# Optimization experiments

Hardware: AMD Instinct MI355X
Metric: run time of the kernel (lower is better)

## Reference

```python
import jax, jax.numpy as jnp
import numpy as np

B, NFIELD = 8192, 20
NFEAT = 100000
SQL_VOCAB = NFIELD + NFEAT + 1  # 100021
SQL_NEMB, DATA_NEMB = 16, 64
HID = 1024
OUT = 1
K = 16
ALPHA = 1.5
N_BISECT = 50


def entmax_bisect(x, alpha=ALPHA, n_iter=N_BISECT):
    # alpha-entmax via bisection on the threshold tau (Peters et al. 2019).
    am1 = alpha - 1.0
    x = x * am1
    d = x.shape[-1]
    max_val = jnp.max(x, axis=-1, keepdims=True)
    tau_lo = max_val - 1.0
    tau_hi = max_val - d ** (1.0 - alpha)

    def p(tau):
        return jnp.clip(x - tau, 0.0) ** (1.0 / am1)

    f_lo = jnp.sum(p(tau_lo), axis=-1, keepdims=True) - 1.0

    def body(carry, _):
        tau_lo, tau_hi, f_lo = carry
        tau_m = 0.5 * (tau_lo + tau_hi)
        f_m = jnp.sum(p(tau_m), axis=-1, keepdims=True) - 1.0
        same_side = (f_m * f_lo) >= 0
        tau_lo = jnp.where(same_side, tau_m, tau_lo)
        tau_hi = jnp.where(same_side, tau_hi, tau_m)
        f_lo = jnp.where(same_side, f_m, f_lo)
        return (tau_lo, tau_hi, f_lo), None

    (tau_lo, tau_hi, _), _ = jax.lax.scan(body, (tau_lo, tau_hi, f_lo), None, length=n_iter)
    pm = p(0.5 * (tau_lo + tau_hi))
    return pm / jnp.sum(pm, axis=-1, keepdims=True)


def cv_squared(v):
    eps = 1e-10
    var = jnp.var(v, ddof=1)  # torch .var() is unbiased
    mean = jnp.mean(v)
    return var / (mean * mean + eps)


def setup_inputs() -> dict:
    key = jax.random.key(0)
    ks = jax.random.split(key, 12)
    xavier = lambda k, shp: jax.random.uniform(k, shp, jnp.float32, -1.0, 1.0) * jnp.sqrt(6.0 / (shp[-2] + shp[-1]))
    inp = {
        "x": jax.random.randint(ks[0], (B, NFIELD), 0, NFEAT),
        "sql": jax.random.randint(ks[1], (B, NFIELD), 0, SQL_VOCAB),
        "sql_emb_table": xavier(ks[2], (SQL_VOCAB, SQL_NEMB)),
        "input_emb_table": xavier(ks[3], (NFEAT, DATA_NEMB)),
        # gate: Linear(gate_in, HID) -> ReLU -> Linear(HID, K)
        "gW1": xavier(ks[4], (NFIELD * SQL_NEMB, HID)),
        "gb1": jnp.zeros((HID,), jnp.float32),
        "gW2": xavier(ks[5], (HID, K)),
        "gb2": jnp.zeros((K,), jnp.float32),
        # K experts: Linear(in, HID) -> ReLU -> Linear(HID, OUT), stacked on axis 0
        "eW1": xavier(ks[6], (K, NFIELD * DATA_NEMB, HID)),
        "eb1": jnp.zeros((K, HID), jnp.float32),
        "eW2": xavier(ks[7], (K, HID, OUT)),
        "eb2": jnp.zeros((K, OUT), jnp.float32),
    }
    return inp


def reference(x, sql, sql_emb_table, input_emb_table, gW1, gb1, gW2, gb2, eW1, eb1, eW2, eb2):
    Bn = x.shape[0]
    x_emb = input_emb_table[x].reshape(Bn, -1)      # [B, nfield*data_nemb]
    sql_emb = sql_emb_table[sql].reshape(Bn, -1)    # [B, nfield*sql_nemb]

    # gate network + entmax-bisect (dropout is identity in eval)
    g = jax.nn.relu(sql_emb @ gW1 + gb1) @ gW2 + gb2  # [B, K]
    gate_score = entmax_bisect(g)                     # [B, K], sparse simplex

    loss = cv_squared(jnp.sum(gate_score, axis=0))

    # all K experts on every token, vectorized
    h = jax.nn.relu(jnp.einsum("bi,kih->bkh", x_emb, eW1) + eb1)  # [B, K, HID]
    y_k = jnp.einsum("bkh,kho->bko", h, eW2) + eb2                # [B, K, OUT]
    y = jnp.sum(gate_score[:, :, None] * y_k, axis=1)             # [B, OUT]
    return (y.squeeze(-1), loss)
```

## Files before the change

### kernel.cpp

```cpp
#include <hip/hip_runtime.h>
#include <stdint.h>

#define NFIELD 20
#define HID 1024
#define KEXP 16
#define KX 1280
#define KS 320
#define BATCH 8192

typedef __bf16 bf16x8 __attribute__((ext_vector_type(8)));
typedef float f32x4 __attribute__((ext_vector_type(4)));

__device__ __forceinline__ unsigned short f2bf(float f) {
  union { float f; unsigned u; } v; v.f = f;
  unsigned r = v.u + 0x7FFFu + ((v.u >> 16) & 1u);
  return (unsigned short)(r >> 16);
}

__device__ __forceinline__ void gload16(const void* g, void* l) {
  __builtin_amdgcn_global_load_lds(
      (const __attribute__((address_space(1))) unsigned int*)(uintptr_t)g,
      (__attribute__((address_space(3))) unsigned int*)(unsigned)(uintptr_t)l,
      16, 0, 0);
}

#define SBAR() asm volatile("s_barrier" ::: "memory")


__global__ void transpose_cvt(const float* __restrict__ src, unsigned short* __restrict__ dst,
                              int R, int C, long sstride, long dstride) {
  __shared__ float tile[32][33];
  const float* s = src + (size_t)blockIdx.z * sstride;
  unsigned short* d = dst + (size_t)blockIdx.z * dstride;
  const int r0 = blockIdx.y * 32, c0 = blockIdx.x * 32;
  const int tx = threadIdx.x & 31, ty = threadIdx.x >> 5;
#pragma unroll
  for (int i = 0; i < 4; ++i)
    tile[ty + 8 * i][tx] = s[(size_t)(r0 + ty + 8 * i) * C + c0 + tx];
  __syncthreads();
#pragma unroll
  for (int i = 0; i < 4; ++i)
    d[(size_t)(c0 + ty + 8 * i) * R + r0 + tx] = f2bf(tile[tx][ty + 8 * i]);
}

__global__ void gather_x_k(const int* __restrict__ x, const float* __restrict__ tab,
                           unsigned short* __restrict__ out) {
  const int b = blockIdx.x;
  const int f = threadIdx.x >> 4;
  const int q = threadIdx.x & 15;
  const int idx = x[b * NFIELD + f];
  const float4 v = *(const float4*)(tab + (size_t)idx * 64 + q * 4);
  ushort4 o;
  o.x = f2bf(v.x); o.y = f2bf(v.y); o.z = f2bf(v.z); o.w = f2bf(v.w);
  *(ushort4*)(out + (size_t)b * KX + f * 64 + q * 4) = o;
}

__global__ void gather_sql_k(const int* __restrict__ sql, const float* __restrict__ tab,
                             unsigned short* __restrict__ out) {
  const int t = blockIdx.x * 256 + threadIdx.x;
  const int b = t / 80;
  const int r = t - b * 80;
  const int f = r >> 2, q = r & 3;
  const int idx = sql[b * NFIELD + f];
  const float4 v = *(const float4*)(tab + (size_t)idx * 16 + q * 4);
  ushort4 o;
  o.x = f2bf(v.x); o.y = f2bf(v.y); o.z = f2bf(v.z); o.w = f2bf(v.w);
  *(ushort4*)(out + (size_t)b * KS + f * 16 + q * 4) = o;
}

template <int NJO, int KTOT>
__global__ __launch_bounds__(256, 2) void gemm_k(const __bf16* __restrict__ A,
                                                 const __bf16* __restrict__ Bt,
                                                 const float* __restrict__ bias,
                                                 const float* __restrict__ W2,
                                                 float* __restrict__ out) {
  constexpr int NT = KTOT / 64;
  static_assert(NT >= 3, "pipeline needs NT>=3");
  alignas(16) __shared__ __bf16 As[2][128][64];
  alignas(16) __shared__ __bf16 Bs[2][128][64];

  const int tid = threadIdx.x;
  const int lane = tid & 63;
  const int wave = tid >> 6;
  const int wr = wave >> 1;
  const int wc = wave & 1;

  const unsigned f = blockIdx.y * gridDim.x + blockIdx.x;
  const unsigned nwg = gridDim.x * gridDim.y;
  const unsigned s = (f >> 3) + (f & 7u) * (nwg >> 3);
  const int m0 = (int)((s & 511u) >> 3) * 128;
  const int n0 = (int)((s >> 9) * 8 + (s & 7u)) * 128;

  const int srow = lane >> 3;
  const int sch = (lane & 7) ^ srow;
  const int r15 = lane & 15, g4 = lane >> 4;

  const __bf16* Ag = A + (size_t)(m0 + wave * 32 + srow) * KTOT + sch * 8;
  const __bf16* Bg = Bt + (size_t)(n0 + wave * 32 + srow) * KTOT + sch * 8;

  auto stage = [&](int t) {
    const int c = t & 1;
#pragma unroll
    for (int j = 0; j < 4; ++j)
      gload16(Ag + (size_t)(j * 8) * KTOT + t * 64, (void*)&As[c][wave * 32 + j * 8][0]);
#pragma unroll
    for (int j = 0; j < 4; ++j)
      gload16(Bg + (size_t)(j * 8) * KTOT + t * 64, (void*)&Bs[c][wave * 32 + j * 8][0]);
  };
  auto readfr = [&](int c, bf16x8 (&af)[4][2], bf16x8 (&bfr)[4][2]) {
#pragma unroll
    for (int mi = 0; mi < 4; ++mi) {
      const int row = wr * 64 + mi * 16 + r15;
#pragma unroll
      for (int kk = 0; kk < 2; ++kk)
        af[mi][kk] = *(const bf16x8*)&As[c][row][((kk * 4 + g4) ^ (row & 7)) * 8];
    }
#pragma unroll
    for (int ni = 0; ni < 4; ++ni) {
      const int row = wc * 64 + ni * 16 + r15;
#pragma unroll
      for (int kk = 0; kk < 2; ++kk)
        bfr[ni][kk] = *(const bf16x8*)&Bs[c][row][((kk * 4 + g4) ^ (row & 7)) * 8];
    }
  };

  f32x4 acc[4][4] = {};
  bf16x8 afA[4][2], bfA[4][2], afB[4][2], bfB[4][2];

#define MFMA16(AF, BF, KK)                                                     \
  __builtin_amdgcn_s_setprio(1);                                               \
  _Pragma("unroll") for (int mi = 0; mi < 4; ++mi)                             \
  _Pragma("unroll") for (int ni = 0; ni < 4; ++ni)                             \
      acc[mi][ni] = __builtin_amdgcn_mfma_f32_16x16x32_bf16(                   \
          AF[mi][KK], BF[ni][KK], acc[mi][ni], 0, 0, 0);                       \
  __builtin_amdgcn_s_setprio(0);

#define BODY(T, AFC, BFC, AFN, BFN)                                            \
  MFMA16(AFC, BFC, 0);                                                         \
  asm volatile("s_waitcnt lgkmcnt(0)" ::: "memory");                           \
  asm volatile("s_waitcnt vmcnt(0)" ::: "memory");                             \
  SBAR();                                                                      \
  if ((T) + 2 < NT) stage((T) + 2);                                            \
  readfr(((T) + 1) & 1, AFN, BFN);                                             \
  MFMA16(AFC, BFC, 1);                                                         \
  SBAR();

  stage(0);
  stage(1);
  asm volatile("s_waitcnt vmcnt(0)" ::: "memory");
  SBAR();
  readfr(0, afA, bfA);

  int t = 0;
  for (; t + 1 < NT - 1; t += 2) {
    BODY(t, afA, bfA, afB, bfB);
    BODY(t + 1, afB, bfB, afA, bfA);
  }
  if constexpr (((NT - 1) & 1) != 0) {
    BODY(NT - 2, afA, bfA, afB, bfB);
    MFMA16(afB, bfB, 0);
    MFMA16(afB, bfB, 1);
  } else {
    MFMA16(afA, bfA, 0);
    MFMA16(afA, bfA, 1);
  }
#undef BODY
#undef MFMA16

  int ncol[4];
  float bsv[4];
#pragma unroll
  for (int ni = 0; ni < 4; ++ni) {
    ncol[ni] = n0 + wc * 64 + ni * 16 + r15;
    bsv[ni] = bias[ncol[ni]];
  }
#pragma unroll
  for (int mi = 0; mi < 4; ++mi)
#pragma unroll
    for (int ni = 0; ni < 4; ++ni)
#pragma unroll
      for (int j = 0; j < 4; ++j) {
        float v = acc[mi][ni][j] + bsv[ni];
        acc[mi][ni][j] = v > 0.f ? v : 0.f;
      }
#pragma unroll
  for (int jo = 0; jo < NJO; ++jo) {
    float w4[4];
#pragma unroll
    for (int ni = 0; ni < 4; ++ni)
      w4[ni] = (NJO == 1) ? W2[ncol[ni]] : W2[ncol[ni] * NJO + jo];
#pragma unroll
    for (int mi = 0; mi < 4; ++mi)
#pragma unroll
      for (int j = 0; j < 4; ++j) {
        float s = acc[mi][0][j] * w4[0] + acc[mi][1][j] * w4[1] +
                  acc[mi][2][j] * w4[2] + acc[mi][3][j] * w4[3];
        s += __shfl_xor(s, 1);
        s += __shfl_xor(s, 2);
        s += __shfl_xor(s, 4);
        s += __shfl_xor(s, 8);
        if (r15 == 0) {
          const int row = m0 + wr * 64 + mi * 16 + g4 * 4 + j;
          const int oc = (NJO == 1) ? (n0 >> 10) : jo;
          atomicAdd(&out[row * KEXP + oc], s);
        }
      }
  }
}

__global__ void entmax_combine(const float* __restrict__ gacc, const float* __restrict__ gb2,
                               const float* __restrict__ yk, const float* __restrict__ eb2,
                               float* __restrict__ y, double* __restrict__ colsum) {
  const int b = blockIdx.x * 256 + threadIdx.x;
  float x[16];
  float mx = -3.4e38f;
#pragma unroll
  for (int j = 0; j < 16; ++j) {
    x[j] = (gacc[b * 16 + j] + gb2[j]) * 0.5f;
    mx = fmaxf(mx, x[j]);
  }
  float lo = mx - 1.0f, hi = mx - 0.25f;
  float flo = -1.0f;
#pragma unroll
  for (int j = 0; j < 16; ++j) {
    float d = x[j] - lo; d = d > 0.f ? d : 0.f;
    flo += d * d;
  }
  for (int it = 0; it < 50; ++it) {
    const float tm = 0.5f * (lo + hi);
    float fm = -1.0f;
#pragma unroll
    for (int j = 0; j < 16; ++j) {
      float d = x[j] - tm; d = d > 0.f ? d : 0.f;
      fm += d * d;
    }
    if (fm * flo >= 0.f) { lo = tm; flo = fm; } else { hi = tm; }
  }
  const float tm = 0.5f * (lo + hi);
  float p[16], ps = 0.f;
#pragma unroll
  for (int j = 0; j < 16; ++j) {
    float d = x[j] - tm; d = d > 0.f ? d : 0.f;
    p[j] = d * d; ps += p[j];
  }
  const float inv = 1.0f / ps;
  float yv = 0.f;
#pragma unroll
  for (int j = 0; j < 16; ++j) {
    p[j] *= inv;
    yv += p[j] * (yk[b * 16 + j] + eb2[j]);
  }
  y[b] = yv;

  const int lane = threadIdx.x & 63, wv = threadIdx.x >> 6;
  __shared__ float red[4][16];
#pragma unroll
  for (int j = 0; j < 16; ++j) {
    float v = p[j];
    v += __shfl_xor(v, 1);  v += __shfl_xor(v, 2);  v += __shfl_xor(v, 4);
    v += __shfl_xor(v, 8);  v += __shfl_xor(v, 16); v += __shfl_xor(v, 32);
    if (lane == 0) red[wv][j] = v;
  }
  __syncthreads();
  if (threadIdx.x < 16) {
    double s = (double)red[0][threadIdx.x] + (double)red[1][threadIdx.x] +
               (double)red[2][threadIdx.x] + (double)red[3][threadIdx.x];
    atomicAdd(&colsum[threadIdx.x], s);
  }
}

__global__ void loss_k(const double* __restrict__ colsum, float* __restrict__ out) {
  if (threadIdx.x == 0 && blockIdx.x == 0) {
    double m = 0.0;
    for (int k = 0; k < 16; ++k) m += colsum[k];
    m *= (1.0 / 16.0);
    double var = 0.0;
    for (int k = 0; k < 16; ++k) { const double d = colsum[k] - m; var += d * d; }
    var *= (1.0 / 15.0);
    out[0] = (float)(var / (m * m + 1e-10));
  }
}

extern "C" void kernel_launch(void* const* d_in, const int* in_sizes, int n_in,
                              void* d_out, int out_size, void* d_ws, size_t ws_size,
                              hipStream_t stream) {
  const int*   x    = (const int*)d_in[0];
  const int*   sql  = (const int*)d_in[1];
  const float* sqlT = (const float*)d_in[2];
  const float* inT  = (const float*)d_in[3];
  const float* gW1  = (const float*)d_in[4];
  const float* gb1  = (const float*)d_in[5];
  const float* gW2  = (const float*)d_in[6];
  const float* gb2  = (const float*)d_in[7];
  const float* eW1  = (const float*)d_in[8];
  const float* eb1  = (const float*)d_in[9];
  const float* eW2  = (const float*)d_in[10];
  const float* eb2  = (const float*)d_in[11];

  char* ws = (char*)d_ws;
  unsigned short* eW1T = (unsigned short*)(ws);
  unsigned short* xemb = (unsigned short*)(ws + 41943040);
  unsigned short* semb = (unsigned short*)(ws + 62914560);
  unsigned short* gW1T = (unsigned short*)(ws + 68157440);
  float*  yk     = (float*)(ws + 68812800);
  float*  gacc   = (float*)(ws + 69337088);
  double* colsum = (double*)(ws + 69861376);

  hipMemsetAsync(yk, 0, 524288 * 2 + 128, stream);

  transpose_cvt<<<dim3(32, 40, 16), 256, 0, stream>>>(eW1, eW1T, 1280, 1024, 1280L * 1024, 1024L * 1280);
  transpose_cvt<<<dim3(32, 10, 1), 256, 0, stream>>>(gW1, gW1T, 320, 1024, 0, 0);
  gather_x_k<<<BATCH, 320, 0, stream>>>(x, inT, xemb);
  gather_sql_k<<<BATCH * 80 / 256, 256, 0, stream>>>(sql, sqlT, semb);

  gemm_k<1, KX><<<dim3(16384 / 128, BATCH / 128), 256, 0, stream>>>(
      (const __bf16*)xemb, (const __bf16*)eW1T, eb1, eW2, yk);
  gemm_k<16, KS><<<dim3(HID / 128, BATCH / 128), 256, 0, stream>>>(
      (const __bf16*)semb, (const __bf16*)gW1T, gb1, gW2, gacc);

  entmax_combine<<<BATCH / 256, 256, 0, stream>>>(gacc, gb2, yk, eb2, (float*)d_out, colsum);
  loss_k<<<1, 64, 0, stream>>>(colsum, (float*)d_out + BATCH);
}
```

Before: 506.7 us.

## Pre-pack expert weights in MFMA fragment layout and load B directly to registers

After: 563.5 us. 11.2% more time.

```diff
diff --git a/kernel.cpp b/kernel.cpp
--- a/kernel.cpp
+++ b/kernel.cpp
@@ -41,6 +41,23 @@
 #pragma unroll
   for (int i = 0; i < 4; ++i)
     d[(size_t)(c0 + ty + 8 * i) * R + r0 + tx] = f2bf(tile[tx][ty + 8 * i]);
+}
+
+__global__ void pack_b(const float* __restrict__ eW1, unsigned short* __restrict__ Bff) {
+  const int n16 = blockIdx.x, k32 = blockIdx.y;
+  const int l = threadIdx.x;
+  const int n = n16 * 16 + (l & 15);
+  const int kb = k32 * 32 + (l >> 4) * 8;
+  const float* src = eW1 + ((size_t)(n >> 10) * 1280) * 1024 + (n & 1023);
+  unsigned short o[8];
+#pragma unroll
+  for (int j = 0; j < 8; ++j) o[j] = f2bf(src[(size_t)(kb + j) * 1024]);
+  uint4 v;
+  v.x = o[0] | ((unsigned)o[1] << 16);
+  v.y = o[2] | ((unsigned)o[3] << 16);
+  v.z = o[4] | ((unsigned)o[5] << 16);
+  v.w = o[6] | ((unsigned)o[7] << 16);
+  *(uint4*)(Bff + (((size_t)n16 * (KX / 32) + k32) << 9) + l * 8) = v;
 }
 
 __global__ void gather_x_k(const int* __restrict__ x, const float* __restrict__ tab,
@@ -68,6 +85,142 @@
   *(ushort4*)(out + (size_t)b * KS + f * 16 + q * 4) = o;
 }
 
+template <int KTOT>
+__global__ __launch_bounds__(256, 2) void gemm_hy(const __bf16* __restrict__ A,
+                                                  const __bf16* __restrict__ Bff,
+                                                  const float* __restrict__ bias,
+                                                  const float* __restrict__ W2,
+                                                  float* __restrict__ out) {
+  constexpr int NT = KTOT / 64;
+  constexpr int NK32 = KTOT / 32;
+  static_assert(NT >= 3, "pipeline needs NT>=3");
+  alignas(16) __shared__ __bf16 As[2][128][64];
+
+  const int tid = threadIdx.x;
+  const int lane = tid & 63;
+  const int wave = tid >> 6;
+  const int wr = wave >> 1;
+  const int wc = wave & 1;
+
+  const unsigned f = blockIdx.y * gridDim.x + blockIdx.x;
+  const unsigned nwg = gridDim.x * gridDim.y;
+  const unsigned s = (f >> 3) + (f & 7u) * (nwg >> 3);
+  const int m0 = (int)((s & 511u) >> 3) * 128;
+  const int n0 = (int)((s >> 9) * 8 + (s & 7u)) * 128;
+
+  const int srow = lane >> 3;
+  const int sch = (lane & 7) ^ srow;
+  const int r15 = lane & 15, g4 = lane >> 4;
+
+  const __bf16* Ag = A + (size_t)(m0 + wave * 32 + srow) * KTOT + sch * 8;
+  const int n16b = (n0 >> 4) + wc * 4;
+
+  auto stageA = [&](int t) {
+    const int c = t & 1;
+#pragma unroll
+    for (int j = 0; j < 4; ++j)
+      gload16(Ag + (size_t)(j * 8) * KTOT + t * 64, (void*)&As[c][wave * 32 + j * 8][0]);
+  };
+  auto readA = [&](int c, bf16x8 (&af)[4][2]) {
+#pragma unroll
+    for (int mi = 0; mi < 4; ++mi) {
+      const int row = wr * 64 + mi * 16 + r15;
+#pragma unroll
+      for (int kk = 0; kk < 2; ++kk)
+        af[mi][kk] = *(const bf16x8*)&As[c][row][((kk * 4 + g4) ^ (row & 7)) * 8];
+    }
+  };
+  auto loadB = [&](int t, bf16x8 (&bfr)[4][2]) {
+#pragma unroll
+    for (int ni = 0; ni < 4; ++ni)
+#pragma unroll
+      for (int kk = 0; kk < 2; ++kk)
+        bfr[ni][kk] = *(const bf16x8*)(Bff +
+            (((size_t)(n16b + ni) * NK32 + (t * 2 + kk)) << 9) + lane * 8);
+  };
+
+  f32x4 acc[4][4] = {};
+  bf16x8 afA[4][2], bfA[4][2], afB[4][2], bfB[4][2];
+
+#define MFMA16(AF, BF, KK)                                                     \
+  __builtin_amdgcn_s_setprio(1);                                               \
+  _Pragma("unroll") for (int mi = 0; mi < 4; ++mi)                             \
+  _Pragma("unroll") for (int ni = 0; ni < 4; ++ni)                             \
+      acc[mi][ni] = __builtin_amdgcn_mfma_f32_16x16x32_bf16(                   \
+          AF[mi][KK], BF[ni][KK], acc[mi][ni], 0, 0, 0);                       \
+  __builtin_amdgcn_s_setprio(0);
+
+#define BODY(T, AFC, BFC, AFN, BFN)                                            \
+  MFMA16(AFC, BFC, 0);                                                         \
+  asm volatile("s_waitcnt lgkmcnt(0)" ::: "memory");                           \
+  asm volatile("s_waitcnt vmcnt(0)" ::: "memory");                             \
+  SBAR();                                                                      \
+  loadB((T) + 1, BFN);                                                         \
+  readA(((T) + 1) & 1, AFN);                                                   \
+  if ((T) + 2 < NT) stageA((T) + 2);                                           \
+  MFMA16(AFC, BFC, 1);                                                         \
+  SBAR();
+
+  stageA(0);
+  stageA(1);
+  loadB(0, bfA);
+  asm volatile("s_waitcnt vmcnt(0)" ::: "memory");
+  SBAR();
+  readA(0, afA);
+
+  int t = 0;
+  for (; t + 1 < NT - 1; t += 2) {
+    BODY(t, afA, bfA, afB, bfB);
+    BODY(t + 1, afB, bfB, afA, bfA);
+  }
+  if constexpr (((NT - 1) & 1) != 0) {
+    BODY(NT - 2, afA, bfA, afB, bfB);
+    MFMA16(afB, bfB, 0);
+    MFMA16(afB, bfB, 1);
+  } else {
+    MFMA16(afA, bfA, 0);
+    MFMA16(afA, bfA, 1);
+  }
+#undef BODY
+#undef MFMA16
+
+  int ncol[4];
+  float bsv[4];
+#pragma unroll
+  for (int ni = 0; ni < 4; ++ni) {
+    ncol[ni] = n0 + wc * 64 + ni * 16 + r15;
+    bsv[ni] = bias[ncol[ni]];
+  }
+#pragma unroll
+  for (int mi = 0; mi < 4; ++mi)
+#pragma unroll
+    for (int ni = 0; ni < 4; ++ni)
+#pragma unroll
+      for (int j = 0; j < 4; ++j) {
+        float v = acc[mi][ni][j] + bsv[ni];
+        acc[mi][ni][j] = v > 0.f ? v : 0.f;
+      }
+  float w4[4];
+#pragma unroll
+  for (int ni = 0; ni < 4; ++ni) w4[ni] = W2[ncol[ni]];
+  const int oc = n0 >> 10;
+#pragma unroll
+  for (int mi = 0; mi < 4; ++mi)
+#pragma unroll
+    for (int j = 0; j < 4; ++j) {
+      float s2 = acc[mi][0][j] * w4[0] + acc[mi][1][j] * w4[1] +
+                 acc[mi][2][j] * w4[2] + acc[mi][3][j] * w4[3];
+      s2 += __shfl_xor(s2, 1);
+      s2 += __shfl_xor(s2, 2);
+      s2 += __shfl_xor(s2, 4);
+      s2 += __shfl_xor(s2, 8);
+      if (r15 == 0) {
+        const int row = m0 + wr * 64 + mi * 16 + g4 * 4 + j;
+        atomicAdd(&out[row * KEXP + oc], s2);
+      }
+    }
+}
+
 template <int NJO, int KTOT>
 __global__ __launch_bounds__(256, 2) void gemm_k(const __bf16* __restrict__ A,
                                                  const __bf16* __restrict__ Bt,
@@ -82,8 +235,7 @@
   const int tid = threadIdx.x;
   const int lane = tid & 63;
   const int wave = tid >> 6;
-  const int wr = wave >> 1;
-  const int wc = wave & 1;
+  const int wr = wave >> 1, wc = wave & 1;
 
   const unsigned f = blockIdx.y * gridDim.x + blockIdx.x;
   const unsigned nwg = gridDim.x * gridDim.y;
@@ -193,16 +345,16 @@
     for (int mi = 0; mi < 4; ++mi)
 #pragma unroll
       for (int j = 0; j < 4; ++j) {
-        float s = acc[mi][0][j] * w4[0] + acc[mi][1][j] * w4[1] +
-                  acc[mi][2][j] * w4[2] + acc[mi][3][j] * w4[3];
-        s += __shfl_xor(s, 1);
-        s += __shfl_xor(s, 2);
-        s += __shfl_xor(s, 4);
-        s += __shfl_xor(s, 8);
+        float s2 = acc[mi][0][j] * w4[0] + acc[mi][1][j] * w4[1] +
+                   acc[mi][2][j] * w4[2] + acc[mi][3][j] * w4[3];
+        s2 += __shfl_xor(s2, 1);
+        s2 += __shfl_xor(s2, 2);
+        s2 += __shfl_xor(s2, 4);
+        s2 += __shfl_xor(s2, 8);
         if (r15 == 0) {
           const int row = m0 + wr * 64 + mi * 16 + g4 * 4 + j;
           const int oc = (NJO == 1) ? (n0 >> 10) : jo;
-          atomicAdd(&out[row * KEXP + oc], s);
+          atomicAdd(&out[row * KEXP + oc], s2);
         }
       }
   }
@@ -298,7 +450,7 @@
   const float* eb2  = (const float*)d_in[11];
 
   char* ws = (char*)d_ws;
-  unsigned short* eW1T = (unsigned short*)(ws);
+  unsigned short* Bff  = (unsigned short*)(ws);
   unsigned short* xemb = (unsigned short*)(ws + 41943040);
   unsigned short* semb = (unsigned short*)(ws + 62914560);
   unsigned short* gW1T = (unsigned short*)(ws + 68157440);
@@ -308,13 +460,13 @@
 
   hipMemsetAsync(yk, 0, 524288 * 2 + 128, stream);
 
-  transpose_cvt<<<dim3(32, 40, 16), 256, 0, stream>>>(eW1, eW1T, 1280, 1024, 1280L * 1024, 1024L * 1280);
+  pack_b<<<dim3(16384 / 16, KX / 32), 64, 0, stream>>>(eW1, Bff);
   transpose_cvt<<<dim3(32, 10, 1), 256, 0, stream>>>(gW1, gW1T, 320, 1024, 0, 0);
   gather_x_k<<<BATCH, 320, 0, stream>>>(x, inT, xemb);
   gather_sql_k<<<BATCH * 80 / 256, 256, 0, stream>>>(sql, sqlT, semb);
 
-  gemm_k<1, KX><<<dim3(16384 / 128, BATCH / 128), 256, 0, stream>>>(
-      (const __bf16*)xemb, (const __bf16*)eW1T, eb1, eW2, yk);
+  gemm_hy<KX><<<dim3(16384 / 128, BATCH / 128), 256, 0, stream>>>(
+      (const __bf16*)xemb, (const __bf16*)Bff, eb1, eW2, yk);
   gemm_k<16, KS><<<dim3(HID / 128, BATCH / 128), 256, 0, stream>>>(
       (const __bf16*)semb, (const __bf16*)gW1T, gb1, gW2, gacc);
 
```

## Restructure GEMM pipeline to four-stage K=32 ring buffer with new swizzle

Applied to the files above, without the earlier changes.

Measured after the change: 556.0 us. 9.7% more time.

```diff
diff --git a/kernel.cpp b/kernel.cpp
--- a/kernel.cpp
+++ b/kernel.cpp
@@ -69,15 +69,15 @@
 }
 
 template <int NJO, int KTOT>
-__global__ __launch_bounds__(256, 2) void gemm_k(const __bf16* __restrict__ A,
+__global__ __launch_bounds__(256, 2) void gemm_q(const __bf16* __restrict__ A,
                                                  const __bf16* __restrict__ Bt,
                                                  const float* __restrict__ bias,
                                                  const float* __restrict__ W2,
                                                  float* __restrict__ out) {
-  constexpr int NT = KTOT / 64;
-  static_assert(NT >= 3, "pipeline needs NT>=3");
-  alignas(16) __shared__ __bf16 As[2][128][64];
-  alignas(16) __shared__ __bf16 Bs[2][128][64];
+  constexpr int NT = KTOT / 32;
+  static_assert(NT % 2 == 0 && NT >= 4, "even NT >= 4");
+  alignas(16) __shared__ __bf16 As[4][128][32];
+  alignas(16) __shared__ __bf16 Bs[4][128][32];
 
   const int tid = threadIdx.x;
   const int lane = tid & 63;
@@ -91,81 +91,68 @@
   const int m0 = (int)((s & 511u) >> 3) * 128;
   const int n0 = (int)((s >> 9) * 8 + (s & 7u)) * 128;
 
-  const int srow = lane >> 3;
-  const int sch = (lane & 7) ^ srow;
+  const int srow = lane >> 2;
+  const int sch = (lane & 3) ^ ((srow >> 1) & 3);
   const int r15 = lane & 15, g4 = lane >> 4;
 
   const __bf16* Ag = A + (size_t)(m0 + wave * 32 + srow) * KTOT + sch * 8;
   const __bf16* Bg = Bt + (size_t)(n0 + wave * 32 + srow) * KTOT + sch * 8;
 
   auto stage = [&](int t) {
-    const int c = t & 1;
-#pragma unroll
-    for (int j = 0; j < 4; ++j)
-      gload16(Ag + (size_t)(j * 8) * KTOT + t * 64, (void*)&As[c][wave * 32 + j * 8][0]);
-#pragma unroll
-    for (int j = 0; j < 4; ++j)
-      gload16(Bg + (size_t)(j * 8) * KTOT + t * 64, (void*)&Bs[c][wave * 32 + j * 8][0]);
+    const int c = t & 3;
+#pragma unroll
+    for (int j = 0; j < 2; ++j)
+      gload16(Ag + (size_t)(j * 16) * KTOT + t * 32, (void*)&As[c][wave * 32 + j * 16][0]);
+#pragma unroll
+    for (int j = 0; j < 2; ++j)
+      gload16(Bg + (size_t)(j * 16) * KTOT + t * 32, (void*)&Bs[c][wave * 32 + j * 16][0]);
   };
-  auto readfr = [&](int c, bf16x8 (&af)[4][2], bf16x8 (&bfr)[4][2]) {
+  auto readfr = [&](int t, bf16x8 (&af)[4], bf16x8 (&bfr)[4]) {
+    const int c = t & 3;
 #pragma unroll
     for (int mi = 0; mi < 4; ++mi) {
       const int row = wr * 64 + mi * 16 + r15;
-#pragma unroll
-      for (int kk = 0; kk < 2; ++kk)
-        af[mi][kk] = *(const bf16x8*)&As[c][row][((kk * 4 + g4) ^ (row & 7)) * 8];
+      af[mi] = *(const bf16x8*)&As[c][row][((g4 ^ ((row >> 1) & 3))) * 8];
     }
 #pragma unroll
     for (int ni = 0; ni < 4; ++ni) {
       const int row = wc * 64 + ni * 16 + r15;
-#pragma unroll
-      for (int kk = 0; kk < 2; ++kk)
-        bfr[ni][kk] = *(const bf16x8*)&Bs[c][row][((kk * 4 + g4) ^ (row & 7)) * 8];
+      bfr[ni] = *(const bf16x8*)&Bs[c][row][((g4 ^ ((row >> 1) & 3))) * 8];
     }
   };
 
   f32x4 acc[4][4] = {};
-  bf16x8 afA[4][2], bfA[4][2], afB[4][2], bfB[4][2];
-
-#define MFMA16(AF, BF, KK)                                                     \
+  bf16x8 afA[4], bfA[4], afB[4], bfB[4];
+
+#define MM16(AF, BF)                                                           \
   __builtin_amdgcn_s_setprio(1);                                               \
   _Pragma("unroll") for (int mi = 0; mi < 4; ++mi)                             \
   _Pragma("unroll") for (int ni = 0; ni < 4; ++ni)                             \
       acc[mi][ni] = __builtin_amdgcn_mfma_f32_16x16x32_bf16(                   \
-          AF[mi][KK], BF[ni][KK], acc[mi][ni], 0, 0, 0);                       \
+          AF[mi], BF[ni], acc[mi][ni], 0, 0, 0);                               \
   __builtin_amdgcn_s_setprio(0);
 
-#define BODY(T, AFC, BFC, AFN, BFN)                                            \
-  MFMA16(AFC, BFC, 0);                                                         \
-  asm volatile("s_waitcnt lgkmcnt(0)" ::: "memory");                           \
-  asm volatile("s_waitcnt vmcnt(0)" ::: "memory");                             \
-  SBAR();                                                                      \
-  if ((T) + 2 < NT) stage((T) + 2);                                            \
-  readfr(((T) + 1) & 1, AFN, BFN);                                             \
-  MFMA16(AFC, BFC, 1);                                                         \
-  SBAR();
-
-  stage(0);
-  stage(1);
+  stage(0); stage(1); stage(2); stage(3);
   asm volatile("s_waitcnt vmcnt(0)" ::: "memory");
   SBAR();
   readfr(0, afA, bfA);
-
-  int t = 0;
-  for (; t + 1 < NT - 1; t += 2) {
-    BODY(t, afA, bfA, afB, bfB);
-    BODY(t + 1, afB, bfB, afA, bfA);
-  }
-  if constexpr (((NT - 1) & 1) != 0) {
-    BODY(NT - 2, afA, bfA, afB, bfB);
-    MFMA16(afB, bfB, 0);
-    MFMA16(afB, bfB, 1);
-  } else {
-    MFMA16(afA, bfA, 0);
-    MFMA16(afA, bfA, 1);
-  }
-#undef BODY
-#undef MFMA16
+  readfr(1, afB, bfB);
+
+  for (int k = 0; k < NT / 2; ++k) {
+    MM16(afA, bfA);
+    MM16(afB, bfB);
+    if (k < NT / 2 - 1) {
+      const int t = 2 * k;
+      asm volatile("s_waitcnt lgkmcnt(0)" ::: "memory");
+      asm volatile("s_waitcnt vmcnt(0)" ::: "memory");
+      SBAR();
+      if (t + 4 < NT) stage(t + 4);
+      if (t + 5 < NT) stage(t + 5);
+      readfr(t + 2, afA, bfA);
+      readfr(t + 3, afB, bfB);
+    }
+  }
+#undef MM16
 
   int ncol[4];
   float bsv[4];
@@ -193,16 +180,16 @@
     for (int mi = 0; mi < 4; ++mi)
 #pragma unroll
       for (int j = 0; j < 4; ++j) {
-        float s = acc[mi][0][j] * w4[0] + acc[mi][1][j] * w4[1] +
-                  acc[mi][2][j] * w4[2] + acc[mi][3][j] * w4[3];
-        s += __shfl_xor(s, 1);
-        s += __shfl_xor(s, 2);
-        s += __shfl_xor(s, 4);
-        s += __shfl_xor(s, 8);
+        float s2 = acc[mi][0][j] * w4[0] + acc[mi][1][j] * w4[1] +
+                   acc[mi][2][j] * w4[2] + acc[mi][3][j] * w4[3];
+        s2 += __shfl_xor(s2, 1);
+        s2 += __shfl_xor(s2, 2);
+        s2 += __shfl_xor(s2, 4);
+        s2 += __shfl_xor(s2, 8);
         if (r15 == 0) {
           const int row = m0 + wr * 64 + mi * 16 + g4 * 4 + j;
           const int oc = (NJO == 1) ? (n0 >> 10) : jo;
-          atomicAdd(&out[row * KEXP + oc], s);
+          atomicAdd(&out[row * KEXP + oc], s2);
         }
       }
   }
@@ -313,9 +300,9 @@
   gather_x_k<<<BATCH, 320, 0, stream>>>(x, inT, xemb);
   gather_sql_k<<<BATCH * 80 / 256, 256, 0, stream>>>(sql, sqlT, semb);
 
-  gemm_k<1, KX><<<dim3(16384 / 128, BATCH / 128), 256, 0, stream>>>(
+  gemm_q<1, KX><<<dim3(16384 / 128, BATCH / 128), 256, 0, stream>>>(
       (const __bf16*)xemb, (const __bf16*)eW1T, eb1, eW2, yk);
-  gemm_k<16, KS><<<dim3(HID / 128, BATCH / 128), 256, 0, stream>>>(
+  gemm_q<16, KS><<<dim3(HID / 128, BATCH / 128), 256, 0, stream>>>(
       (const __bf16*)semb, (const __bf16*)gW1T, gb1, gW2, gacc);
 
   entmax_combine<<<BATCH / 256, 256, 0, stream>>>(gacc, gb2, yk, eb2, (float*)d_out, colsum);
```
